# Kernel tuning notes

Hardware: AMD Instinct MI355X
Metric: run time of the kernel (lower is better)

## Reference

```python
import jax, jax.numpy as jnp
import numpy as np

N_HEADS = 16  # init kwarg n_heads
LN_EPS = 1e-5  # torch LayerNorm default eps


def setup_inputs() -> dict:
    key = jax.random.key(0)
    k1, k2, k3 = jax.random.split(key, 3)
    b, s, d = 4, 2048, 1024
    x0 = jax.random.normal(k1, (b, s, d), dtype=jnp.float32)
    # input_maps['x0']: Linear(d, 3*d, bias=False); stored as (in, out) so x @ W_in
    W_in = jax.random.normal(k2, (d, 3 * d), dtype=jnp.float32) * (d ** -0.5)
    # W_o: Linear(d, d, bias=False)
    W_o = jax.random.normal(k3, (d, d), dtype=jnp.float32) * (d ** -0.5)
    # key-padding mask: True = masked. All-valid (zeros) per spec.
    src_mask = jnp.zeros((b, s), dtype=bool)
    return {"x0": x0, "W_in": W_in, "W_o": W_o, "src_mask": src_mask}


def reference(x0, W_in, W_o, src_mask):
    b, s, d = x0.shape
    dh = d // N_HEADS  # per-head dim after chunking q,k,v
    x = jnp.einsum('bsd,de->bse', x0, W_in)  # (b, s, 3d)
    # rearrange 'b s (n_h 3*dh) -> b s n_h (3*dh)' then chunk into q,k,v
    x = x.reshape(b, s, N_HEADS, 3 * dh)
    q, k, v = jnp.split(x, 3, axis=-1)  # each (b, s, n_h, dh)
    logits = jnp.einsum('bqhd,bkhd->bhqk', q, k) * (dh ** -0.5)  # (b, n_h, s, s)
    causal = jnp.triu(jnp.ones((s, s), dtype=bool), k=1)
    mask = src_mask[:, None, None, :] | causal[None, None, :, :]
    logits = jnp.where(mask, -jnp.inf, logits)
    attn = jax.nn.softmax(logits, axis=-1)
    out = jnp.einsum('bhqk,bkhd->bqhd', attn, v).reshape(b, s, d)
    out = jnp.einsum('bsd,de->bse', out, W_o)
    y = out + x0  # residual with X[input_names[0]]
    # LayerNorm(out_dim, elementwise_affine=False)
    mu = jnp.mean(y, axis=-1, keepdims=True)
    var = jnp.var(y, axis=-1, keepdims=True)
    return (y - mu) * jax.lax.rsqrt(var + LN_EPS)
```

## Files before the change

### kernel.cpp

```cpp
#include <hip/hip_runtime.h>
#include <hip/hip_bf16.h>

typedef unsigned short u16;
typedef unsigned int u32;
typedef __attribute__((ext_vector_type(8))) short short8;
typedef __attribute__((ext_vector_type(4))) float f32x4;
typedef __attribute__((ext_vector_type(4))) int i32x4;

__device__ __forceinline__ float b2f(u16 u) {
    union { u32 i; float f; } x; x.i = ((u32)u) << 16; return x.f;
}
__device__ __forceinline__ u16 f2b(float f) {
    union { float f; u32 u; } x; x.f = f;
    u32 r = x.u + 0x7fffu + ((x.u >> 16) & 1u);
    return (u16)(r >> 16);
}
__device__ __forceinline__ u32 pkbf(float a, float b) {
    union { __hip_bfloat162 h; u32 u; } x;
    x.h = __float22bfloat162_rn(make_float2(a, b));
    return x.u;
}
__device__ __forceinline__ void async_cp16(const u16* g, u16* l) {
    __builtin_amdgcn_global_load_lds(
        (const __attribute__((address_space(1))) void*)g,
        (__attribute__((address_space(3))) void*)l, 16, 0, 0);
}
__device__ __forceinline__ float fexp2(float x) {
#if __has_builtin(__builtin_amdgcn_exp2f)
    return __builtin_amdgcn_exp2f(x);
#else
    return __expf(x * 0.6931471805599453f);
#endif
}
#define L2E 1.44269504f

__global__ __launch_bounds__(256) void canon_all(
    const void* __restrict__ x0src, const void* __restrict__ wiSrc,
    const void* __restrict__ woSrc,
    u16* __restrict__ cx0, u16* __restrict__ wtin, u16* __restrict__ wto,
    int* __restrict__ flagp)
{
    __shared__ __align__(16) u16 t[64 * 72];
    const int tid = threadIdx.x;
    const int bid = blockIdx.x;

    int big = 0;
#pragma unroll
    for (int i = tid; i < 512; i += 256) {
        float v = fabsf(b2f(((const u16*)x0src)[i]));
        if (!(v <= 1e6f)) big = 1;
    }
    const int f = __syncthreads_or(big);
    if (bid == 0 && tid == 0) *flagp = f ? 1 : 0;

    if (bid < 4096) {
        int i = (bid * 256 + tid) * 8;
        if (f) {
            const float* s = (const float*)x0src + i;
            f32x4 a = *(const f32x4*)s;
            f32x4 b = *(const f32x4*)(s + 4);
            union { i32x4 v; u32 w[4]; } o;
            o.w[0] = pkbf(a[0], a[1]); o.w[1] = pkbf(a[2], a[3]);
            o.w[2] = pkbf(b[0], b[1]); o.w[3] = pkbf(b[2], b[3]);
            *(i32x4*)(cx0 + i) = o.v;
        } else {
            *(i32x4*)(cx0 + i) = *(const i32x4*)((const u16*)x0src + i);
        }
        return;
    }

    const void* src; u16* dst; int Mdim, Ndim, m0, n0;
    if (bid < 4096 + 768) {
        int local = bid - 4096;
        src = wiSrc; dst = wtin; Mdim = 1024; Ndim = 3072;
        m0 = (local & 15) * 64; n0 = (local >> 4) * 64;
    } else {
        int local = bid - 4096 - 768;
        src = woSrc; dst = wto; Mdim = 1024; Ndim = 1024;
        m0 = (local & 15) * 64; n0 = (local >> 4) * 64;
    }
#pragma unroll
    for (int p = 0; p < 2; ++p) {
        int s = tid + p * 256;
        int r = s >> 3, c0 = (s & 7) << 3;
        union { i32x4 v; u32 w[4]; } o;
        if (f) {
            const float* sp = (const float*)src + (size_t)(m0 + r) * Ndim + n0 + c0;
            f32x4 a = *(const f32x4*)sp, b = *(const f32x4*)(sp + 4);
            o.w[0] = pkbf(a[0], a[1]); o.w[1] = pkbf(a[2], a[3]);
            o.w[2] = pkbf(b[0], b[1]); o.w[3] = pkbf(b[2], b[3]);
        } else {
            o.v = *(const i32x4*)((const u16*)src + (size_t)(m0 + r) * Ndim + n0 + c0);
        }
        *(i32x4*)(t + r * 72 + c0) = o.v;
    }
    __syncthreads();
#pragma unroll
    for (int p = 0; p < 2; ++p) {
        int s = tid + p * 256;
        int oc = s >> 3, mc = (s & 7) << 3;
        union { i32x4 v; u16 h[8]; } o;
#pragma unroll
        for (int j = 0; j < 8; ++j) o.h[j] = t[(mc + j) * 72 + oc];
        *(i32x4*)(dst + (size_t)(n0 + oc) * Mdim + m0 + mc) = o.v;
    }
}

__global__ __launch_bounds__(256) void vtrans(
    const u16* __restrict__ qkv, u16* __restrict__ vT)
{
    __shared__ __align__(16) u16 t[64 * 72];
    const int bh = blockIdx.x, b = bh >> 4, h = bh & 15;
    const int s0 = blockIdx.y * 64;
    const int tid = threadIdx.x;
#pragma unroll
    for (int p = 0; p < 2; ++p) {
        int s = tid + p * 256;
        int r = s >> 3, c0 = (s & 7) << 3;
        *(i32x4*)(t + r * 72 + c0) =
            *(const i32x4*)(qkv + (size_t)(b * 2048 + s0 + r) * 3072 + h * 192 + 128 + c0);
    }
    __syncthreads();
#pragma unroll
    for (int p = 0; p < 2; ++p) {
        int s = tid + p * 256;
        int oc = s >> 3, mc = (s & 7) << 3;
        union { i32x4 v; u16 h[8]; } o;
#pragma unroll
        for (int j = 0; j < 8; ++j) o.h[j] = t[(mc + j) * 72 + oc];
        *(i32x4*)(vT + (size_t)(h * 64 + oc) * 8192 + b * 2048 + s0 + mc) = o.v;
    }
}

__global__ __launch_bounds__(512, 2) void gemm_bp(
    const u16* __restrict__ A, const u16* __restrict__ Bt, u16* __restrict__ C,
    int M, int N, int K)
{
    __shared__ __align__(16) u16 sA0[256 * 64], sA1[256 * 64], sA2[256 * 64];
    __shared__ __align__(16) u16 sB0[128 * 64], sB1[128 * 64];
    const int tid  = threadIdx.x;
    const int lane = tid & 63;
    const int wave = tid >> 6;
    const int la = lane & 15;
    const int qd = lane >> 4;
    const int wm = wave >> 1;
    const int wn = wave & 1;

    const int x = blockIdx.x & 7;
    const int q = blockIdx.x >> 3;
    const int r = q >> 5;
    const int p = q & 31;
    const int m0 = (x * 4 + (p & 3)) * 256;
    const int n0 = (r * 8 + (p >> 2)) * 128;

    const int srow = tid >> 3;
    const int scol = (((tid & 7) ^ (srow & 7)) << 3);
    const int nt = K >> 6;

    const u16* gA = A  + (size_t)(m0 + srow) * K + scol;
    const u16* gB = Bt + (size_t)(n0 + srow) * K + scol;

    auto stageA = [&](int tk, u16* buf) {
        u16* dst = buf + tid * 8;
        const u16* g = gA + tk * 64;
#pragma unroll
        for (int h = 0; h < 4; ++h)
            async_cp16(g + (size_t)(h * 64) * K, dst + h * 64 * 64);
    };
    auto stageB = [&](int tk, u16* buf) {
        u16* dst = buf + tid * 8;
        const u16* g = gB + tk * 64;
#pragma unroll
        for (int h = 0; h < 2; ++h)
            async_cp16(g + (size_t)(h * 64) * K, dst + h * 64 * 64);
    };

    f32x4 acc[4][4];
    const f32x4 fz = {0.f, 0.f, 0.f, 0.f};
#pragma unroll
    for (int i = 0; i < 4; ++i)
#pragma unroll
        for (int j = 0; j < 4; ++j) acc[i][j] = fz;

    u16 *aCur = sA0, *aNxt = sA1, *aNN = sA2;
    u16 *bCur = sB0, *bNxt = sB1;

    stageA(0, aCur); stageB(0, bCur); stageA(1, aNxt);
    asm volatile("s_waitcnt vmcnt(4)" ::: "memory");
    __builtin_amdgcn_s_barrier();

    const int swk = la & 7;

    for (int t = 0; t < nt; ++t) {
        short8 a0[4], b0[4];
#pragma unroll
        for (int f = 0; f < 4; ++f)
            a0[f] = *(const short8*)(aCur + (wm * 64 + f * 16 + la) * 64 +
                                     ((qd ^ swk) << 3));
#pragma unroll
        for (int f = 0; f < 4; ++f)
            b0[f] = *(const short8*)(bCur + (wn * 64 + f * 16 + la) * 64 +
                                     ((qd ^ swk) << 3));
        if (t + 1 < nt) stageB(t + 1, bNxt);
        if (t + 2 < nt) stageA(t + 2, aNN);
        __builtin_amdgcn_s_barrier();
        asm volatile("s_waitcnt lgkmcnt(0)" ::: "memory");
        __builtin_amdgcn_s_setprio(1);
#pragma unroll
        for (int i = 0; i < 4; ++i)
#pragma unroll
            for (int j = 0; j < 4; ++j)
                acc[i][j] = __builtin_amdgcn_mfma_f32_16x16x32_bf16(
                    a0[i], b0[j], acc[i][j], 0, 0, 0);
        __builtin_amdgcn_s_setprio(0);
        __builtin_amdgcn_s_barrier();

        short8 a1[4], b1[4];
#pragma unroll
        for (int f = 0; f < 4; ++f)
            a1[f] = *(const short8*)(aCur + (wm * 64 + f * 16 + la) * 64 +
                                     (((4 + qd) ^ swk) << 3));
#pragma unroll
        for (int f = 0; f < 4; ++f)
            b1[f] = *(const short8*)(bCur + (wn * 64 + f * 16 + la) * 64 +
                                     (((4 + qd) ^ swk) << 3));
        __builtin_amdgcn_s_barrier();
        asm volatile("s_waitcnt lgkmcnt(0)" ::: "memory");
        __builtin_amdgcn_s_setprio(1);
#pragma unroll
        for (int i = 0; i < 4; ++i)
#pragma unroll
            for (int j = 0; j < 4; ++j)
                acc[i][j] = __builtin_amdgcn_mfma_f32_16x16x32_bf16(
                    a1[i], b1[j], acc[i][j], 0, 0, 0);
        __builtin_amdgcn_s_setprio(0);
        if (t + 2 < nt)      asm volatile("s_waitcnt vmcnt(4)" ::: "memory");
        else if (t + 1 < nt) asm volatile("s_waitcnt vmcnt(0)" ::: "memory");
        __builtin_amdgcn_s_barrier();

        u16* tmp = aCur; aCur = aNxt; aNxt = aNN; aNN = tmp;
        tmp = bCur; bCur = bNxt; bNxt = tmp;
    }

#pragma unroll
    for (int fi = 0; fi < 4; ++fi)
#pragma unroll
        for (int fj = 0; fj < 4; ++fj)
#pragma unroll
            for (int r2 = 0; r2 < 4; ++r2) {
                int row = m0 + wm * 64 + fi * 16 + qd * 4 + r2;
                int col = n0 + wn * 64 + fj * 16 + la;
                C[(size_t)row * N + col] = f2b(acc[fi][fj][r2]);
            }
}

#define S_LEN 2048
#define D3 3072
#define NEG_BIG (-30000.0f)

__global__ __launch_bounds__(256, 4) void attn_fwd(
    const u16* __restrict__ qkv, const u16* __restrict__ vT,
    u16* __restrict__ outp)
{
    __shared__ __align__(16) u16 Ks[2 * 64 * 64];
    __shared__ __align__(16) u16 Vts[2 * 64 * 64];
    __shared__ __align__(16) u16 Ps[64 * 64];
    const int tid  = threadIdx.x;
    const int lane = tid & 63;
    const int wave = tid >> 6;
    const int la = lane & 15;
    const int qd = lane >> 4;
    const int lin = blockIdx.y * 16 + blockIdx.x;
    const int xcd = lin & 7, idx = lin >> 3;
    const int bh = xcd * 8 + (idx >> 4);
    const int px = idx & 15;
    const int b = bh >> 4, h = bh & 15;
    const size_t rowb = (size_t)b * S_LEN * D3;
    const int hq = h * 192;
    const u16* vTp = vT + (size_t)(h * 64) * 8192 + (size_t)b * 2048;
    const f32x4 fz = {0.f, 0.f, 0.f, 0.f};

    const int srow = tid >> 3;
    const int scol = ((tid & 7) ^ (srow & 7)) << 3;
    const u16* gK = qkv + rowb + (size_t)srow * D3 + hq + 64 + scol;
    const u16* gV = vTp + (size_t)srow * 8192 + scol;

    const int swz = (la & 7);

    int cur = 0;
#pragma unroll
    for (int seg = 0; seg < 2; ++seg) {
        const int qt = seg == 0 ? px : 31 - px;
        const int q0 = qt * 64;
        const int qg = q0 + wave * 16 + la;

        short8 bq[2];
#pragma unroll
        for (int s = 0; s < 2; ++s) {
            union { short8 v; u16 h[8]; } u;
            u.v = *(const short8*)(qkv + rowb + (size_t)qg * D3 + hq + s * 32 + qd * 8);
#pragma unroll
            for (int j = 0; j < 8; ++j) u.h[j] = f2b(b2f(u.h[j]) * 0.125f);
            bq[s] = u.v;
        }

        f32x4 Oacc[4];
#pragma unroll
        for (int jd = 0; jd < 4; ++jd) Oacc[jd] = fz;
        float m_run = NEG_BIG, l_part = 0.f;

        __syncthreads();
#pragma unroll
        for (int c = 0; c < 2; ++c) {
            async_cp16(gK + (size_t)(c * 32) * D3, Ks + cur * 4096 + c * 2048 + wave * 512);
            async_cp16(gV + (size_t)(c * 32) * 8192, Vts + cur * 4096 + c * 2048 + wave * 512);
        }

        for (int kt = 0; kt <= qt; ++kt) {
            const int k0 = kt * 64;
            __syncthreads();
            if (kt < qt) {
                const int kn = k0 + 64;
#pragma unroll
                for (int c = 0; c < 2; ++c) {
                    async_cp16(gK + (size_t)(kn + c * 32) * D3,
                               Ks + (cur ^ 1) * 4096 + c * 2048 + wave * 512);
                    async_cp16(gV + (size_t)(c * 32) * 8192 + kn,
                               Vts + (cur ^ 1) * 4096 + c * 2048 + wave * 512);
                }
            }
            const u16* KsC  = Ks  + cur * 4096;
            const u16* VtsC = Vts + cur * 4096;

            f32x4 sacc[4];
#pragma unroll
            for (int jm = 0; jm < 4; ++jm) sacc[jm] = fz;
            __builtin_amdgcn_s_setprio(1);
#pragma unroll
            for (int s = 0; s < 2; ++s) {
#pragma unroll
                for (int jm = 0; jm < 4; ++jm) {
                    short8 ak = *(const short8*)(KsC + (jm * 16 + la) * 64 +
                                                 (((s * 4 + qd) ^ swz) << 3));
                    sacc[jm] = __builtin_amdgcn_mfma_f32_16x16x32_bf16(ak, bq[s], sacc[jm], 0, 0, 0);
                }
            }
            __builtin_amdgcn_s_setprio(0);
            if (kt == qt) {
#pragma unroll
                for (int jm = 0; jm < 4; ++jm)
#pragma unroll
                    for (int r = 0; r < 4; ++r)
                        if (k0 + jm * 16 + qd * 4 + r > qg) sacc[jm][r] = NEG_BIG;
            }

            float g0 = fmaxf(fmaxf(sacc[0][0], sacc[0][1]), sacc[0][2]);
            float g1 = fmaxf(fmaxf(sacc[0][3], sacc[1][0]), sacc[1][1]);
            float g2 = fmaxf(fmaxf(sacc[1][2], sacc[1][3]), sacc[2][0]);
            float g3 = fmaxf(fmaxf(sacc[2][1], sacc[2][2]), sacc[2][3]);
            float g4 = fmaxf(fmaxf(sacc[3][0], sacc[3][1]), sacc[3][2]);
            float mx = fmaxf(fmaxf(fmaxf(g0, g1), g2),
                             fmaxf(fmaxf(g3, g4), sacc[3][3]));
            mx = fmaxf(mx, __shfl_xor(mx, 16));
            mx = fmaxf(mx, __shfl_xor(mx, 32));

            const int skip = __all(mx <= m_run + 4.0f);
            if (!skip) {
                float mnew = fmaxf(m_run, mx);
                float al   = fexp2((m_run - mnew) * L2E);
                float ar[4];
#pragma unroll
                for (int r = 0; r < 4; ++r) ar[r] = __shfl(al, qd * 4 + r);
#pragma unroll
                for (int jd = 0; jd < 4; ++jd)
#pragma unroll
                    for (int r = 0; r < 4; ++r) Oacc[jd][r] *= ar[r];
                l_part *= al;
                m_run = mnew;
            }
            const float nm2 = m_run * L2E;
            float ssum = 0.f;
#pragma unroll
            for (int jm = 0; jm < 4; ++jm)
#pragma unroll
                for (int r = 0; r < 4; ++r) {
                    float pv = fexp2(fmaf(sacc[jm][r], L2E, -nm2));
                    sacc[jm][r] = pv;
                    ssum += pv;
                }
            l_part += ssum;

#pragma unroll
            for (int jm = 0; jm < 4; ++jm) {
                uint2 w;
                w.x = pkbf(sacc[jm][0], sacc[jm][1]);
                w.y = pkbf(sacc[jm][2], sacc[jm][3]);
                *(uint2*)(Ps + (wave * 16 + la) * 64 +
                          ((((jm * 2 + (qd >> 1)) ^ swz)) << 3) + ((qd & 1) << 2)) = w;
            }

            __builtin_amdgcn_s_setprio(1);
#pragma unroll
            for (int s = 0; s < 2; ++s) {
                short8 ap = *(const short8*)(Ps + (wave * 16 + la) * 64 +
                                             (((s * 4 + qd) ^ swz) << 3));
#pragma unroll
                for (int jd = 0; jd < 4; ++jd) {
                    short8 bv = *(const short8*)(VtsC + (jd * 16 + la) * 64 +
                                                 (((s * 4 + qd) ^ swz) << 3));
                    Oacc[jd] = __builtin_amdgcn_mfma_f32_16x16x32_bf16(ap, bv, Oacc[jd], 0, 0, 0);
                }
            }
            __builtin_amdgcn_s_setprio(0);
            cur ^= 1;
        }

        float lt = l_part;
        lt += __shfl_xor(lt, 16);
        lt += __shfl_xor(lt, 32);
#pragma unroll
        for (int r = 0; r < 4; ++r) {
            float lr = __shfl(lt, qd * 4 + r);
            float inv = 1.f / lr;
            size_t orow = (size_t)(b * S_LEN + q0 + wave * 16 + qd * 4 + r) * 1024 + h * 64;
#pragma unroll
            for (int jd = 0; jd < 4; ++jd)
                outp[orow + jd * 16 + la] = f2b(Oacc[jd][r] * inv);
        }
    }
}

__global__ __launch_bounds__(256) void ln_residual(
    const u16* __restrict__ proj, const u16* __restrict__ x0,
    void* __restrict__ out, const int* __restrict__ flag)
{
    __shared__ float red[8];
    __shared__ float stats[2];
    const size_t base = (size_t)blockIdx.x * 1024 + threadIdx.x * 4;
    union { uint2 u; u16 s[4]; } pa, xa;
    pa.u = *(const uint2*)(proj + base);
    xa.u = *(const uint2*)(x0 + base);
    float y[4];
    float s1 = 0.f, s2 = 0.f;
#pragma unroll
    for (int j = 0; j < 4; ++j) {
        y[j] = b2f(pa.s[j]) + b2f(xa.s[j]);
        s1 += y[j];
        s2 += y[j] * y[j];
    }
#pragma unroll
    for (int off = 32; off > 0; off >>= 1) {
        s1 += __shfl_down(s1, off);
        s2 += __shfl_down(s2, off);
    }
    const int wave = threadIdx.x >> 6, lane = threadIdx.x & 63;
    if (lane == 0) { red[wave * 2] = s1; red[wave * 2 + 1] = s2; }
    __syncthreads();
    if (threadIdx.x == 0) {
        float S1 = red[0] + red[2] + red[4] + red[6];
        float S2 = red[1] + red[3] + red[5] + red[7];
        float mean = S1 * (1.f / 1024.f);
        float var  = fmaxf(S2 * (1.f / 1024.f) - mean * mean, 0.f);
        stats[0] = mean;
        stats[1] = rsqrtf(var + 1e-5f);
    }
    __syncthreads();
    float mean = stats[0], inv = stats[1];
    if (*flag) {
        f32x4 o;
#pragma unroll
        for (int j = 0; j < 4; ++j) o[j] = (y[j] - mean) * inv;
        *(f32x4*)((float*)out + base) = o;
    } else {
        union { uint2 u; u16 s[4]; } o;
#pragma unroll
        for (int j = 0; j < 4; ++j) o.s[j] = f2b((y[j] - mean) * inv);
        *(uint2*)((u16*)out + base) = o.u;
    }
}

extern "C" void kernel_launch(void* const* d_in, const int* in_sizes, int n_in,
                              void* d_out, int out_size, void* d_ws, size_t ws_size,
                              hipStream_t stream) {
    char* ws = (char*)d_ws;
    int* flag = (int*)ws;
    u16* cx0  = (u16*)(ws + 256);
    u16* wtin = cx0  + (size_t)8192 * 1024;
    u16* wto  = wtin + (size_t)3072 * 1024;
    u16* qkv  = wto  + (size_t)1024 * 1024;
    u16* vT   = qkv  + (size_t)8192 * 3072;
    u16* attn = vT   + (size_t)1024 * 8192;
    u16* proj = qkv;

    dim3 blk(256);
    canon_all<<<dim3(4096 + 768 + 256), blk, 0, stream>>>(
        d_in[0], d_in[1], d_in[2], cx0, wtin, wto, flag);
    gemm_bp<<<dim3(768), dim3(512), 0, stream>>>(cx0, wtin, qkv, 8192, 3072, 1024);
    vtrans<<<dim3(64, 32), blk, 0, stream>>>(qkv, vT);
    attn_fwd<<<dim3(16, 64), blk, 0, stream>>>(qkv, vT, attn);
    gemm_bp<<<dim3(256), dim3(512), 0, stream>>>(attn, wto, proj, 8192, 1024, 1024);
    ln_residual<<<dim3(8192), blk, 0, stream>>>(proj, cx0, d_out, flag);
}
```

Before: 269.9 us.

## Use 128-row query tiles in attention and a finer-grained GEMM pipeline

The attention kernel now runs 512-thread blocks covering 128 query rows (8 waves), so each K/V tile staged in LDS serves twice as many queries. The grid is halved and the causal pairing is remapped to 128-row units. The projection GEMM drops its triple-buffered A in favour of two LDS buffers, and splits each K step into four smaller MFMA phases with fewer live fragment registers. The aim is less K/V reload traffic, lower register and LDS pressure, and better occupancy. The cost is more barriers per iteration, and the A prefetch now lands in a buffer that is two steps ahead with only double buffering, which risks a hazard.

```diff
diff --git a/kernel.cpp b/kernel.cpp
--- a/kernel.cpp
+++ b/kernel.cpp
@@ -132,12 +132,12 @@
     }
 }
 
-__global__ __launch_bounds__(512, 2) void gemm_bp(
+__global__ __launch_bounds__(512, 2) void gemm_bp8(
     const u16* __restrict__ A, const u16* __restrict__ Bt, u16* __restrict__ C,
     int M, int N, int K)
 {
-    __shared__ __align__(16) u16 sA0[256 * 64], sA1[256 * 64], sA2[256 * 64];
-    __shared__ __align__(16) u16 sB0[128 * 64], sB1[128 * 64];
+    __shared__ __align__(16) u16 sA[2][256 * 64];
+    __shared__ __align__(16) u16 sB[2][128 * 64];
     const int tid  = threadIdx.x;
     const int lane = tid & 63;
     const int wave = tid >> 6;
@@ -160,19 +160,19 @@
     const u16* gA = A  + (size_t)(m0 + srow) * K + scol;
     const u16* gB = Bt + (size_t)(n0 + srow) * K + scol;
 
-    auto stageA = [&](int tk, u16* buf) {
-        u16* dst = buf + tid * 8;
+    auto stageA = [&](int tk) {
+        u16* dst = &sA[tk & 1][0] + tid * 8;
         const u16* g = gA + tk * 64;
 #pragma unroll
         for (int h = 0; h < 4; ++h)
-            async_cp16(g + (size_t)(h * 64) * K, dst + h * 64 * 64);
+            async_cp16(g + (size_t)(h * 64) * K, dst + h * 4096);
     };
-    auto stageB = [&](int tk, u16* buf) {
-        u16* dst = buf + tid * 8;
+    auto stageB = [&](int tk) {
+        u16* dst = &sB[tk & 1][0] + tid * 8;
         const u16* g = gB + tk * 64;
 #pragma unroll
         for (int h = 0; h < 2; ++h)
-            async_cp16(g + (size_t)(h * 64) * K, dst + h * 64 * 64);
+            async_cp16(g + (size_t)(h * 64) * K, dst + h * 4096);
     };
 
     f32x4 acc[4][4];
@@ -182,64 +182,92 @@
 #pragma unroll
         for (int j = 0; j < 4; ++j) acc[i][j] = fz;
 
-    u16 *aCur = sA0, *aNxt = sA1, *aNN = sA2;
-    u16 *bCur = sB0, *bNxt = sB1;
-
-    stageA(0, aCur); stageB(0, bCur); stageA(1, aNxt);
+    stageA(0); stageB(0); stageA(1);
     asm volatile("s_waitcnt vmcnt(4)" ::: "memory");
     __builtin_amdgcn_s_barrier();
 
     const int swk = la & 7;
 
     for (int t = 0; t < nt; ++t) {
-        short8 a0[4], b0[4];
-#pragma unroll
-        for (int f = 0; f < 4; ++f)
-            a0[f] = *(const short8*)(aCur + (wm * 64 + f * 16 + la) * 64 +
+        const u16* pA = &sA[t & 1][0];
+        const u16* pB = &sB[t & 1][0];
+        short8 af[4], bf[2];
+
+#pragma unroll
+        for (int i = 0; i < 4; ++i)
+            af[i] = *(const short8*)(pA + (wm * 64 + i * 16 + la) * 64 +
                                      ((qd ^ swk) << 3));
 #pragma unroll
-        for (int f = 0; f < 4; ++f)
-            b0[f] = *(const short8*)(bCur + (wn * 64 + f * 16 + la) * 64 +
+        for (int f = 0; f < 2; ++f)
+            bf[f] = *(const short8*)(pB + (wn * 64 + f * 16 + la) * 64 +
                                      ((qd ^ swk) << 3));
-        if (t + 1 < nt) stageB(t + 1, bNxt);
-        if (t + 2 < nt) stageA(t + 2, aNN);
+        if (t + 1 < nt) stageB(t + 1);
         __builtin_amdgcn_s_barrier();
         asm volatile("s_waitcnt lgkmcnt(0)" ::: "memory");
         __builtin_amdgcn_s_setprio(1);
 #pragma unroll
         for (int i = 0; i < 4; ++i)
 #pragma unroll
-            for (int j = 0; j < 4; ++j)
-                acc[i][j] = __builtin_amdgcn_mfma_f32_16x16x32_bf16(
-                    a0[i], b0[j], acc[i][j], 0, 0, 0);
+            for (int f = 0; f < 2; ++f)
+                acc[i][f] = __builtin_amdgcn_mfma_f32_16x16x32_bf16(
+                    af[i], bf[f], acc[i][f], 0, 0, 0);
         __builtin_amdgcn_s_setprio(0);
         __builtin_amdgcn_s_barrier();
 
-        short8 a1[4], b1[4];
-#pragma unroll
-        for (int f = 0; f < 4; ++f)
-            a1[f] = *(const short8*)(aCur + (wm * 64 + f * 16 + la) * 64 +
-                                     (((4 + qd) ^ swk) << 3));
-#pragma unroll
-        for (int f = 0; f < 4; ++f)
-            b1[f] = *(const short8*)(bCur + (wn * 64 + f * 16 + la) * 64 +
-                                     (((4 + qd) ^ swk) << 3));
+#pragma unroll
+        for (int f = 0; f < 2; ++f)
+            bf[f] = *(const short8*)(pB + (wn * 64 + (2 + f) * 16 + la) * 64 +
+                                     ((qd ^ swk) << 3));
         __builtin_amdgcn_s_barrier();
         asm volatile("s_waitcnt lgkmcnt(0)" ::: "memory");
         __builtin_amdgcn_s_setprio(1);
 #pragma unroll
         for (int i = 0; i < 4; ++i)
 #pragma unroll
-            for (int j = 0; j < 4; ++j)
-                acc[i][j] = __builtin_amdgcn_mfma_f32_16x16x32_bf16(
-                    a1[i], b1[j], acc[i][j], 0, 0, 0);
+            for (int f = 0; f < 2; ++f)
+                acc[i][2 + f] = __builtin_amdgcn_mfma_f32_16x16x32_bf16(
+                    af[i], bf[f], acc[i][2 + f], 0, 0, 0);
+        __builtin_amdgcn_s_setprio(0);
+        __builtin_amdgcn_s_barrier();
+
+#pragma unroll
+        for (int i = 0; i < 4; ++i)
+            af[i] = *(const short8*)(pA + (wm * 64 + i * 16 + la) * 64 +
+                                     (((4 + qd) ^ swk) << 3));
+#pragma unroll
+        for (int f = 0; f < 2; ++f)
+            bf[f] = *(const short8*)(pB + (wn * 64 + f * 16 + la) * 64 +
+                                     (((4 + qd) ^ swk) << 3));
+        __builtin_amdgcn_s_barrier();
+        asm volatile("s_waitcnt lgkmcnt(0)" ::: "memory");
+        __builtin_amdgcn_s_setprio(1);
+#pragma unroll
+        for (int i = 0; i < 4; ++i)
+#pragma unroll
+            for (int f = 0; f < 2; ++f)
+                acc[i][f] = __builtin_amdgcn_mfma_f32_16x16x32_bf16(
+                    af[i], bf[f], acc[i][f], 0, 0, 0);
+        __builtin_amdgcn_s_setprio(0);
+        __builtin_amdgcn_s_barrier();
+
+#pragma unroll
+        for (int f = 0; f < 2; ++f)
+            bf[f] = *(const short8*)(pB + (wn * 64 + (2 + f) * 16 + la) * 64 +
+                                     (((4 + qd) ^ swk) << 3));
+        if (t + 2 < nt) stageA(t + 2);
+        __builtin_amdgcn_s_barrier();
+        asm volatile("s_waitcnt lgkmcnt(0)" ::: "memory");
+        __builtin_amdgcn_s_setprio(1);
+#pragma unroll
+        for (int i = 0; i < 4; ++i)
+#pragma unroll
+            for (int f = 0; f < 2; ++f)
+                acc[i][2 + f] = __builtin_amdgcn_mfma_f32_16x16x32_bf16(
+                    af[i], bf[f], acc[i][2 + f], 0, 0, 0);
         __builtin_amdgcn_s_setprio(0);
         if (t + 2 < nt)      asm volatile("s_waitcnt vmcnt(4)" ::: "memory");
         else if (t + 1 < nt) asm volatile("s_waitcnt vmcnt(0)" ::: "memory");
         __builtin_amdgcn_s_barrier();
-
-        u16* tmp = aCur; aCur = aNxt; aNxt = aNN; aNN = tmp;
-        tmp = bCur; bCur = bNxt; bNxt = tmp;
     }
 
 #pragma unroll
@@ -258,22 +286,22 @@
 #define D3 3072
 #define NEG_BIG (-30000.0f)
 
-__global__ __launch_bounds__(256, 4) void attn_fwd(
+__global__ __launch_bounds__(512, 4) void attn_fwd(
     const u16* __restrict__ qkv, const u16* __restrict__ vT,
     u16* __restrict__ outp)
 {
     __shared__ __align__(16) u16 Ks[2 * 64 * 64];
     __shared__ __align__(16) u16 Vts[2 * 64 * 64];
-    __shared__ __align__(16) u16 Ps[64 * 64];
+    __shared__ __align__(16) u16 Ps[128 * 64];
     const int tid  = threadIdx.x;
     const int lane = tid & 63;
     const int wave = tid >> 6;
     const int la = lane & 15;
     const int qd = lane >> 4;
-    const int lin = blockIdx.y * 16 + blockIdx.x;
+    const int lin = blockIdx.y * 8 + blockIdx.x;
     const int xcd = lin & 7, idx = lin >> 3;
-    const int bh = xcd * 8 + (idx >> 4);
-    const int px = idx & 15;
+    const int bh = xcd * 8 + (idx >> 3);
+    const int px = idx & 7;
     const int b = bh >> 4, h = bh & 15;
     const size_t rowb = (size_t)b * S_LEN * D3;
     const int hq = h * 192;
@@ -290,9 +318,9 @@
     int cur = 0;
 #pragma unroll
     for (int seg = 0; seg < 2; ++seg) {
-        const int qt = seg == 0 ? px : 31 - px;
-        const int q0 = qt * 64;
-        const int qg = q0 + wave * 16 + la;
+        const int qtU = seg == 0 ? 2 * px + 1 : 31 - 2 * px;
+        const int q0  = (qtU - 1) * 64;
+        const int qg  = q0 + wave * 16 + la;
 
         short8 bq[2];
 #pragma unroll
@@ -310,24 +338,16 @@
         float m_run = NEG_BIG, l_part = 0.f;
 
         __syncthreads();
-#pragma unroll
-        for (int c = 0; c < 2; ++c) {
-            async_cp16(gK + (size_t)(c * 32) * D3, Ks + cur * 4096 + c * 2048 + wave * 512);
-            async_cp16(gV + (size_t)(c * 32) * 8192, Vts + cur * 4096 + c * 2048 + wave * 512);
-        }
-
-        for (int kt = 0; kt <= qt; ++kt) {
+        async_cp16(gK, Ks + cur * 4096 + tid * 8);
+        async_cp16(gV, Vts + cur * 4096 + tid * 8);
+
+        for (int kt = 0; kt <= qtU; ++kt) {
             const int k0 = kt * 64;
             __syncthreads();
-            if (kt < qt) {
+            if (kt < qtU) {
                 const int kn = k0 + 64;
-#pragma unroll
-                for (int c = 0; c < 2; ++c) {
-                    async_cp16(gK + (size_t)(kn + c * 32) * D3,
-                               Ks + (cur ^ 1) * 4096 + c * 2048 + wave * 512);
-                    async_cp16(gV + (size_t)(c * 32) * 8192 + kn,
-                               Vts + (cur ^ 1) * 4096 + c * 2048 + wave * 512);
-                }
+                async_cp16(gK + (size_t)kn * D3, Ks + (cur ^ 1) * 4096 + tid * 8);
+                async_cp16(gV + kn, Vts + (cur ^ 1) * 4096 + tid * 8);
             }
             const u16* KsC  = Ks  + cur * 4096;
             const u16* VtsC = Vts + cur * 4096;
@@ -346,7 +366,7 @@
                 }
             }
             __builtin_amdgcn_s_setprio(0);
-            if (kt == qt) {
+            if (kt + 1 >= qtU) {
 #pragma unroll
                 for (int jm = 0; jm < 4; ++jm)
 #pragma unroll
@@ -495,9 +515,9 @@
     dim3 blk(256);
     canon_all<<<dim3(4096 + 768 + 256), blk, 0, stream>>>(
         d_in[0], d_in[1], d_in[2], cx0, wtin, wto, flag);
-    gemm_bp<<<dim3(768), dim3(512), 0, stream>>>(cx0, wtin, qkv, 8192, 3072, 1024);
+    gemm_bp8<<<dim3(768), dim3(512), 0, stream>>>(cx0, wtin, qkv, 8192, 3072, 1024);
     vtrans<<<dim3(64, 32), blk, 0, stream>>>(qkv, vT);
-    attn_fwd<<<dim3(16, 64), blk, 0, stream>>>(qkv, vT, attn);
-    gemm_bp<<<dim3(256), dim3(512), 0, stream>>>(attn, wto, proj, 8192, 1024, 1024);
+    attn_fwd<<<dim3(8, 64), dim3(512), 0, stream>>>(qkv, vT, attn);
+    gemm_bp8<<<dim3(256), dim3(512), 0, stream>>>(attn, wto, proj, 8192, 1024, 1024);
     ln_residual<<<dim3(8192), blk, 0, stream>>>(proj, cx0, d_out, flag);
 }
```

Measured after the change: 281.1 us. 1.04x slower.
